# Performance work log

Hardware: AMD Instinct MI355X
Metric: run time of the kernel (lower is better)

The kernel has to match this reference:

```python
import jax, jax.numpy as jnp
import numpy as np
import math

LIMBS = [(5, 7), (7, 9), (6, 8), (8, 10), (11, 13), (13, 15), (12, 14), (14, 16), (5, 6), (11, 12), (5, 11), (6, 12), (5, 12), (6, 11)]
PARENT = jnp.array([l[0] for l in LIMBS], dtype=jnp.int32)
CHILD = jnp.array([l[1] for l in LIMBS], dtype=jnp.int32)
EXPECTED_2D_LEN = 0.15

B = 65536
D_MODEL = 64
HID = 128


def _ln(x, g, b, eps=1e-5):
    m = jnp.mean(x, axis=-1, keepdims=True)
    v = jnp.mean(jnp.square(x - m), axis=-1, keepdims=True)
    return (x - m) * jax.lax.rsqrt(v + eps) * g + b


def _unit(x, eps=1e-6):
    # F.normalize semantics: divide by max(norm, eps)
    n = jnp.linalg.norm(x, axis=-1, keepdims=True)
    return x / jnp.maximum(n, eps)


def setup_inputs() -> dict:
    key = jax.random.key(0)
    ks = jax.random.split(key, 32)
    d = {}
    d["joint_features"] = jax.random.normal(ks[0], (B, 17, D_MODEL), jnp.float32)
    d["pose_2d"] = jax.random.normal(ks[1], (B, 17, 2), jnp.float32)
    d["pose_3d"] = jax.random.normal(ks[2], (B, 17, 3), jnp.float32)
    d["azimuth"] = jax.random.uniform(ks[3], (B,), jnp.float32) * 360.0
    d["elevation"] = jax.random.uniform(ks[4], (B,), jnp.float32) * 180.0 - 90.0
    d["projected_2d"] = jax.random.normal(ks[5], (B, 17, 2), jnp.float32)

    def lin(k, out_f, in_f, std=None):
        s = std if std is not None else 1.0 / math.sqrt(in_f)
        return jax.random.normal(k, (out_f, in_f), jnp.float32) * s

    # current_orient_encoder: Linear(3->32), LayerNorm(32), ReLU
    d["co_w"] = lin(ks[6], HID // 4, 3)
    d["co_b"] = jnp.zeros((HID // 4,), jnp.float32)
    d["co_g"] = jnp.ones((HID // 4,), jnp.float32)
    d["co_be"] = jnp.zeros((HID // 4,), jnp.float32)
    # limb_2d_encoder: Linear(4->64), LayerNorm(64), ReLU
    d["l2_w"] = lin(ks[7], HID // 2, 4)
    d["l2_b"] = jnp.zeros((HID // 2,), jnp.float32)
    d["l2_g"] = jnp.ones((HID // 2,), jnp.float32)
    d["l2_be"] = jnp.zeros((HID // 2,), jnp.float32)
    # view_encoder: Linear(7->32), ReLU
    d["v_w"] = lin(ks[8], HID // 4, 7)
    d["v_b"] = jnp.zeros((HID // 4,), jnp.float32)
    # limb_head: Linear(256->128), LN(128), LeakyReLU, Linear(128->128), LeakyReLU, Linear(128->3)
    in_dim = HID // 2 + HID // 4 + D_MODEL * 2 + HID // 4  # 256
    d["h1_w"] = lin(ks[9], HID, in_dim)
    d["h1_b"] = jnp.zeros((HID,), jnp.float32)
    d["h_g"] = jnp.ones((HID,), jnp.float32)
    d["h_be"] = jnp.zeros((HID,), jnp.float32)
    d["h2_w"] = lin(ks[10], HID, HID)
    d["h2_b"] = jnp.zeros((HID,), jnp.float32)
    d["h3_w"] = lin(ks[11], 3, HID, std=0.01)
    d["h3_b"] = jnp.zeros((3,), jnp.float32)
    return d


def reference(joint_features, pose_2d, pose_3d, azimuth, elevation, projected_2d,
              co_w, co_b, co_g, co_be, l2_w, l2_b, l2_g, l2_be, v_w, v_b,
              h1_w, h1_b, h_g, h_be, h2_w, h2_b, h3_w, h3_b):
    nl = PARENT.shape[0]  # 14
    # gather parent/child joint features: (B, 14, d_model)
    pf = joint_features[:, PARENT, :]
    cf = joint_features[:, CHILD, :]
    # current 3D orientations from input pose
    cur = _unit(pose_3d[:, CHILD, :] - pose_3d[:, PARENT, :])  # (B,14,3)
    co = jax.nn.relu(_ln(jnp.einsum('blk,ok->blo', cur, co_w) + co_b, co_g, co_be))
    # view encoder from azimuth/elevation
    az = azimuth * (math.pi / 180.0)
    el = elevation * (math.pi / 180.0)
    sa, ca, se, ce = jnp.sin(az), jnp.cos(az), jnp.sin(el), jnp.cos(el)
    view_in = jnp.stack([sa * ce, se, ca * ce, sa, ca, se, ce], axis=-1)  # (B,7)
    vf = jax.nn.relu(view_in @ v_w.T + v_b)  # (B,32)
    vf = jnp.broadcast_to(vf[:, None, :], (vf.shape[0], nl, vf.shape[-1]))
    # 2D foreshortening features from projected_2d
    v2 = projected_2d[:, CHILD, :] - projected_2d[:, PARENT, :]  # (B,14,2)
    L = jnp.linalg.norm(v2, axis=-1, keepdims=True)
    d2 = v2 / (L + 1e-6)
    ratio = L / (EXPECTED_2D_LEN + 1e-6)
    feat2d = jnp.concatenate([d2, L, ratio], axis=-1)  # (B,14,4)
    l2 = jax.nn.relu(_ln(jnp.einsum('blk,ok->blo', feat2d, l2_w) + l2_b, l2_g, l2_be))
    # concat all branches: (B,14,256)
    lf = jnp.concatenate([l2, co, pf, cf, vf], axis=-1)
    # 3-layer MLP head
    h = jax.nn.leaky_relu(_ln(jnp.einsum('blk,ok->blo', lf, h1_w) + h1_b, h_g, h_be), 0.2)
    h = jax.nn.leaky_relu(jnp.einsum('blk,ok->blo', h, h2_w) + h2_b, 0.2)
    delta = jnp.einsum('blk,ok->blo', h, h3_w) + h3_b  # (B,14,3)
    return _unit(cur + delta)
```

## Files before the change

kernel.cpp:

```cpp
#include <hip/hip_runtime.h>


#define NTHR   1024
#define NBLK   256
#define NTILES 14336
#define C2D    6.66662222251852f
#define RAD    0.017453292519943295f

typedef __bf16 bf16x8 __attribute__((ext_vector_type(8)));
typedef __bf16 bf16x4 __attribute__((ext_vector_type(4)));
typedef float  f32x4  __attribute__((ext_vector_type(4)));

#define PARENT_PK 0x10106097863120ull
#define CHILD_PK  0x677671b9a85342ull

__global__ __launch_bounds__(256) void prep_kernel(
    const float* __restrict__ w1, const float* __restrict__ w2,
    __bf16* __restrict__ wsb)
{
  const int u = blockIdx.x * 256 + threadIdx.x;
  if (u < 4096) {
    const int lane = u & 63, t = u >> 6;
    const int f = t & 1, kk = (t >> 1) & 7, wn = t >> 4;
    const int col = wn * 32 + f * 16 + (lane & 15);
    const int kb  = kk * 32 + (lane >> 4) * 8;
    __bf16* dst = wsb + (size_t)u * 8;
    #pragma unroll
    for (int j = 0; j < 8; ++j) dst[j] = (__bf16)w1[col * 256 + kb + j];
  } else if (u < 6144) {
    const int v = u - 4096;
    const int lane = v & 63, t = v >> 6;
    const int f = t & 1, kk = (t >> 1) & 3, wn = t >> 3;
    const int col = wn * 32 + f * 16 + (lane & 15);
    const int kb  = kk * 32 + (lane >> 4) * 8;
    __bf16* dst = wsb + 32768 + (size_t)v * 8;
    #pragma unroll
    for (int j = 0; j < 8; ++j) dst[j] = (__bf16)w2[col * 128 + kb + j];
  }
}

struct Smem {
  __bf16 w1f[32768];
  __bf16 w2f[16384];
  __bf16 lf[64][264];
  __bf16 h [64][132];
  f32x4  scal4[256];
  float  w3c[384];
  float  h1b[128], hg[128], hbe[128], h2b[128];
  float  partG1[512];
  float  partG2[768];
};

__device__ __forceinline__ float RFL(float x) {
  return __uint_as_float((unsigned)__builtin_amdgcn_readfirstlane((int)__float_as_uint(x)));
}

__global__ __launch_bounds__(NTHR, 4) void limb_kernel(
    const float* __restrict__ jf,  const float* __restrict__ p3g,
    const float* __restrict__ az,  const float* __restrict__ el,
    const float* __restrict__ p2d,
    const float* __restrict__ cow, const float* __restrict__ cob,
    const float* __restrict__ cog, const float* __restrict__ cobe,
    const float* __restrict__ l2w, const float* __restrict__ l2b,
    const float* __restrict__ l2g, const float* __restrict__ l2be,
    const float* __restrict__ vw,  const float* __restrict__ vb,
    const float* __restrict__ h1bg, const float* __restrict__ hgg,
    const float* __restrict__ hbeg, const float* __restrict__ h2bg,
    const float* __restrict__ w3,  const float* __restrict__ h3bg,
    const __bf16* __restrict__ wsb,
    float* __restrict__ out)
{
  __shared__ Smem sm;
  const int tid  = threadIdx.x;
  const int wave = tid >> 6;
  const int lane = tid & 63;
  const int lrow = lane & 15, lk8 = lane >> 4;
  const int mp = wave >> 2, nt = wave & 3;
  const int nrow = nt * 16 + lrow;
  const int cb0 = mp * 32 + lk8 * 4;
  const int cb1 = cb0 + 16;
  const int myrow0 = wave * 4;

  {
    const uint4* s1 = (const uint4*)wsb;
    uint4* d1 = (uint4*)sm.w1f;
    for (int i = tid; i < 4096; i += NTHR) d1[i] = s1[i];
    const uint4* s2 = (const uint4*)(wsb + 32768);
    uint4* d2 = (uint4*)sm.w2f;
    for (int i = tid; i < 2048; i += NTHR) d2[i] = s2[i];
  }
  if (tid < 384) sm.w3c[tid] = w3[tid];
  if (tid < 128) {
    sm.h1b[tid] = h1bg[tid]; sm.hg[tid] = hgg[tid];
    sm.hbe[tid] = hbeg[tid]; sm.h2b[tid] = h2bg[tid];
  }
  const float h3b0 = h3bg[0], h3b1 = h3bg[1], h3b2 = h3bg[2];

  float lQxx, lQxy2, lQxz2, lQyy, lQyz2, lQzz, lrx2, lry2, lrz2, ls0;
  float lmx, lmy, lmz, lmb;
  {
    float s1x = 0, s1y = 0, s1z = 0, sb = 0;
    float sxx = 0, sxy = 0, sxz = 0, syy = 0, syz = 0, szz = 0;
    float sbx = 0, sby = 0, sbz = 0, sbb = 0;
    for (int o = 0; o < 64; ++o) {
      const float w0 = l2w[o * 4 + 0], w1v = l2w[o * 4 + 1];
      const float w2v = l2w[o * 4 + 2] + C2D * l2w[o * 4 + 3];
      const float bo = l2b[o];
      s1x += w0; s1y += w1v; s1z += w2v; sb += bo;
      sxx += w0 * w0; sxy += w0 * w1v; sxz += w0 * w2v;
      syy += w1v * w1v; syz += w1v * w2v; szz += w2v * w2v;
      sbx += w0 * bo; sby += w1v * bo; sbz += w2v * bo; sbb += bo * bo;
    }
    const float i = 1.f / 64.f;
    lmx = RFL(s1x * i); lmy = RFL(s1y * i); lmz = RFL(s1z * i); lmb = RFL(sb * i);
    lQxx = RFL(sxx * i - lmx * lmx); lQxy2 = RFL(2.f * (sxy * i - lmx * lmy));
    lQxz2 = RFL(2.f * (sxz * i - lmx * lmz)); lQyy = RFL(syy * i - lmy * lmy);
    lQyz2 = RFL(2.f * (syz * i - lmy * lmz)); lQzz = RFL(szz * i - lmz * lmz);
    lrx2 = RFL(2.f * (sbx * i - lmx * lmb)); lry2 = RFL(2.f * (sby * i - lmy * lmb));
    lrz2 = RFL(2.f * (sbz * i - lmz * lmb)); ls0 = RFL(sbb * i - lmb * lmb);
  }
  float cQxx, cQxy2, cQxz2, cQyy, cQyz2, cQzz, crx2, cry2, crz2, cs0;
  float cmx, cmy, cmz, cmb;
  {
    float s1x = 0, s1y = 0, s1z = 0, sb = 0;
    float sxx = 0, sxy = 0, sxz = 0, syy = 0, syz = 0, szz = 0;
    float sbx = 0, sby = 0, sbz = 0, sbb = 0;
    for (int o = 0; o < 32; ++o) {
      const float w0 = cow[o * 3 + 0], w1v = cow[o * 3 + 1], w2v = cow[o * 3 + 2];
      const float bo = cob[o];
      s1x += w0; s1y += w1v; s1z += w2v; sb += bo;
      sxx += w0 * w0; sxy += w0 * w1v; sxz += w0 * w2v;
      syy += w1v * w1v; syz += w1v * w2v; szz += w2v * w2v;
      sbx += w0 * bo; sby += w1v * bo; sbz += w2v * bo; sbb += bo * bo;
    }
    const float i = 1.f / 32.f;
    cmx = RFL(s1x * i); cmy = RFL(s1y * i); cmz = RFL(s1z * i); cmb = RFL(sb * i);
    cQxx = RFL(sxx * i - cmx * cmx); cQxy2 = RFL(2.f * (sxy * i - cmx * cmy));
    cQxz2 = RFL(2.f * (sxz * i - cmx * cmz)); cQyy = RFL(syy * i - cmy * cmy);
    cQyz2 = RFL(2.f * (syz * i - cmy * cmz)); cQzz = RFL(szz * i - cmz * cmz);
    crx2 = RFL(2.f * (sbx * i - cmx * cmb)); cry2 = RFL(2.f * (sby * i - cmy * cmb));
    crz2 = RFL(2.f * (sbz * i - cmz * cmb)); cs0 = RFL(sbb * i - cmb * cmb);
  }

  const float lwc0 = l2w[lane * 4 + 0] - lmx;
  const float lwc1 = l2w[lane * 4 + 1] - lmy;
  const float lwc2 = (l2w[lane * 4 + 2] + C2D * l2w[lane * 4 + 3]) - lmz;
  const float lbc  = l2b[lane] - lmb;
  const float lgv  = l2g[lane], lbev = l2be[lane];
  float u0, u1, u2, u3, u4, u5, u6;
  if (lane < 32) {
    u0 = cow[lane * 3 + 0] - cmx; u1 = cow[lane * 3 + 1] - cmy;
    u2 = cow[lane * 3 + 2] - cmz; u3 = cob[lane] - cmb;
    u4 = cog[lane]; u5 = cobe[lane]; u6 = 0.f;
  } else {
    const int o = lane - 32;
    u0 = vw[o * 7 + 0]; u1 = vw[o * 7 + 1] + vw[o * 7 + 5];
    u2 = vw[o * 7 + 2]; u3 = vw[o * 7 + 3];
    u4 = vw[o * 7 + 4]; u5 = vw[o * 7 + 6]; u6 = vb[o];
  }

  auto jf_src = [&](int rg0x, int round) -> const float* {
    const int task = wave * 8 + round * 4 + lk8;
    const int row = task >> 1, half = task & 1;
    const unsigned rg = (unsigned)(rg0x + row);
    const unsigned b = rg / 14u;
    const int l = (int)(rg - b * 14u);
    const int j = half ? 5 + (int)((CHILD_PK >> (4 * l)) & 15ull)
                       : 5 + (int)((PARENT_PK >> (4 * l)) & 15ull);
    return jf + ((size_t)b * 17 + (size_t)j) * 64 + lrow * 4;
  };
  auto jf_store = [&](int round, float4 v) {
    const int task = wave * 8 + round * 4 + lk8;
    const int row = task >> 1, half = task & 1;
    bf16x4 o; o[0] = (__bf16)v.x; o[1] = (__bf16)v.y; o[2] = (__bf16)v.z; o[3] = (__bf16)v.w;
    *(bf16x4*)&sm.lf[row][(half ? 160 : 96) + lrow * 4] = o;
  };
  struct G12 { float p3p0, p3p1, p3p2, p3c0, p3c1, p3c2, q2p0, q2p1, q2c0, q2c1, sazv, selv; };
  auto gather12_row = [&](int rgl) -> G12 {
    G12 g;
    const unsigned rg = (unsigned)rgl;
    const unsigned b = rg / 14u;
    const int l = (int)(rg - b * 14u);
    const int p = 5 + (int)((PARENT_PK >> (4 * l)) & 15ull);
    const int c = 5 + (int)((CHILD_PK  >> (4 * l)) & 15ull);
    const float* p3 = p3g + (size_t)b * 51;
    g.p3p0 = p3[p * 3 + 0]; g.p3p1 = p3[p * 3 + 1]; g.p3p2 = p3[p * 3 + 2];
    g.p3c0 = p3[c * 3 + 0]; g.p3c1 = p3[c * 3 + 1]; g.p3c2 = p3[c * 3 + 2];
    const float* q2 = p2d + (size_t)b * 34;
    g.q2p0 = q2[p * 2 + 0]; g.q2p1 = q2[p * 2 + 1];
    g.q2c0 = q2[c * 2 + 0]; g.q2c1 = q2[c * 2 + 1];
    g.sazv = az[b]; g.selv = el[b];
    return g;
  };
  auto scal_write = [&](int row, const G12& g) {
    const float dx = g.p3c0 - g.p3p0, dy = g.p3c1 - g.p3p1, dz = g.p3c2 - g.p3p2;
    const float ci = 1.f / fmaxf(sqrtf(dx * dx + dy * dy + dz * dz), 1e-6f);
    const float cx = dx * ci, cy = dy * ci, cz = dz * ci;
    const float vx = g.q2c0 - g.q2p0, vy = g.q2c1 - g.q2p1;
    const float L  = sqrtf(vx * vx + vy * vy);
    const float il = 1.f / (L + 1e-6f);
    const float f0 = vx * il, f1 = vy * il;
    const float azr = g.sazv * RAD, elr = g.selv * RAD;
    const float sa = __sinf(azr), ca = __cosf(azr);
    const float se = __sinf(elr), ce = __cosf(elr);
    const float vl = lQxx * f0 * f0 + lQyy * f1 * f1 + lQzz * L * L +
                     lQxy2 * f0 * f1 + lQxz2 * f0 * L + lQyz2 * f1 * L +
                     lrx2 * f0 + lry2 * f1 + lrz2 * L + ls0;
    const float vc = cQxx * cx * cx + cQyy * cy * cy + cQzz * cz * cz +
                     cQxy2 * cx * cy + cQxz2 * cx * cz + cQyz2 * cy * cz +
                     crx2 * cx + cry2 * cy + crz2 * cz + cs0;
    f32x4 s0; s0[0] = cx; s0[1] = cy; s0[2] = cz; s0[3] = f0;
    f32x4 s1; s1[0] = f1; s1[1] = L; s1[2] = rsqrtf(vl + 1e-5f); s1[3] = rsqrtf(vc + 1e-5f);
    f32x4 s2; s2[0] = sa * ce; s2[1] = se; s2[2] = ca * ce; s2[3] = sa;
    f32x4 s3; s3[0] = ca; s3[1] = ce; s3[2] = 0.f; s3[3] = 0.f;
    sm.scal4[row * 4 + 0] = s0; sm.scal4[row * 4 + 1] = s1;
    sm.scal4[row * 4 + 2] = s2; sm.scal4[row * 4 + 3] = s3;
  };
  auto expandB = [&]() {
    #pragma unroll
    for (int rr = 0; rr < 4; ++rr) {
      const int row = myrow0 + rr;
      const f32x4 s0 = sm.scal4[row * 4 + 0];
      const f32x4 s1 = sm.scal4[row * 4 + 1];
      const f32x4 s2 = sm.scal4[row * 4 + 2];
      const f32x4 s3 = sm.scal4[row * 4 + 3];
      {
        const float a = lwc0 * s0[3] + lwc1 * s1[0] + lwc2 * s1[1] + lbc;
        sm.lf[row][lane] = (__bf16)fmaxf(a * s1[2] * lgv + lbev, 0.f);
      }
      if (lane < 32) {
        const float a = u0 * s0[0] + u1 * s0[1] + u2 * s0[2] + u3;
        sm.lf[row][64 + lane] = (__bf16)fmaxf(a * s1[3] * u4 + u5, 0.f);
      } else {
        const float a = u0 * s2[0] + u1 * s2[1] + u2 * s2[2] + u3 * s2[3] +
                        u4 * s3[0] + u5 * s3[1] + u6;
        sm.lf[row][224 + (lane - 32)] = (__bf16)fmaxf(a, 0.f);
      }
    }
  };

  {
    const int rg0 = blockIdx.x * 64;
    jf_store(0, *(const float4*)jf_src(rg0, 0));
    jf_store(1, *(const float4*)jf_src(rg0, 1));
    if (lane < 4) scal_write(myrow0 + lane, gather12_row(rg0 + myrow0 + lane));
    expandB();
  }
  __syncthreads();

  float curx = 0.f, cury = 0.f, curz = 0.f;
  int prevT = -1;

  for (int tile = blockIdx.x; tile < NTILES; tile += NBLK) {
    const int ntile = tile + NBLK;
    const bool pv = ntile < NTILES;

    float4 jva = {0.f, 0.f, 0.f, 0.f}, jvb = jva;
    G12 g = {};
    if (pv) {
      jva = *(const float4*)jf_src(ntile * 64, 0);
      jvb = *(const float4*)jf_src(ntile * 64, 1);
      if (lane < 4) g = gather12_row(ntile * 64 + myrow0 + lane);
    }
    if (prevT >= 0 && lane < 4) {
      const int r = myrow0 + lane;
      const f32x4 q0 = *(const f32x4*)&sm.partG2[r * 12];
      const f32x4 q1 = *(const f32x4*)&sm.partG2[r * 12 + 4];
      const f32x4 q2 = *(const f32x4*)&sm.partG2[r * 12 + 8];
      const float ox = curx + q0[0] + q0[1] + q0[2] + q0[3] + h3b0;
      const float oy = cury + q1[0] + q1[1] + q1[2] + q1[3] + h3b1;
      const float oz = curz + q2[0] + q2[1] + q2[2] + q2[3] + h3b2;
      const float nn = sqrtf(ox * ox + oy * oy + oz * oz);
      const float iv = 1.f / fmaxf(nn, 1e-6f);
      const size_t o0 = (size_t)(prevT * 64 + r) * 3;
      out[o0 + 0] = ox * iv; out[o0 + 1] = oy * iv; out[o0 + 2] = oz * iv;
    }
    f32x4 a0 = {0.f, 0.f, 0.f, 0.f}, a1 = a0;
    #pragma unroll
    for (int kk = 0; kk < 8; ++kk) {
      const bf16x8 fb  = *(const bf16x8*)&sm.lf[nrow][kk * 32 + lk8 * 8];
      const bf16x8 fa0 = *(const bf16x8*)&sm.w1f[(((mp * 8 + kk) * 2 + 0) * 64 + lane) * 8];
      const bf16x8 fa1 = *(const bf16x8*)&sm.w1f[(((mp * 8 + kk) * 2 + 1) * 64 + lane) * 8];
      a0 = __builtin_amdgcn_mfma_f32_16x16x32_bf16(fa0, fb, a0, 0, 0, 0);
      a1 = __builtin_amdgcn_mfma_f32_16x16x32_bf16(fa1, fb, a1, 0, 0, 0);
    }
    const f32x4 hb0 = *(const f32x4*)&sm.h1b[cb0];
    const f32x4 hb1 = *(const f32x4*)&sm.h1b[cb1];
    float v0[4], v1[4], ss = 0.f, qq = 0.f;
    #pragma unroll
    for (int j = 0; j < 4; ++j) {
      v0[j] = a0[j] + hb0[j]; v1[j] = a1[j] + hb1[j];
      ss += v0[j] + v1[j];
      qq = fmaf(v0[j], v0[j], qq); qq = fmaf(v1[j], v1[j], qq);
    }
    ss += __shfl_xor(ss, 16, 64); ss += __shfl_xor(ss, 32, 64);
    qq += __shfl_xor(qq, 16, 64); qq += __shfl_xor(qq, 32, 64);
    if (lk8 == 0) *(float2*)&sm.partG1[nrow * 8 + mp * 2] = make_float2(ss, qq);
    __syncthreads();

    {
      const f32x4 pa = *(const f32x4*)&sm.partG1[nrow * 8];
      const f32x4 pb = *(const f32x4*)&sm.partG1[nrow * 8 + 4];
      const float mean = (pa[0] + pa[2] + pb[0] + pb[2]) * (1.f / 128.f);
      const float var  = (pa[1] + pa[3] + pb[1] + pb[3]) * (1.f / 128.f) - mean * mean;
      const float rs = rsqrtf(var + 1e-5f);
      const f32x4 g0 = *(const f32x4*)&sm.hg[cb0],  g1 = *(const f32x4*)&sm.hg[cb1];
      const f32x4 e0 = *(const f32x4*)&sm.hbe[cb0], e1 = *(const f32x4*)&sm.hbe[cb1];
      bf16x4 y0, y1;
      #pragma unroll
      for (int j = 0; j < 4; ++j) {
        float t0 = (v0[j] - mean) * rs * g0[j] + e0[j]; t0 = (t0 > 0.f) ? t0 : 0.2f * t0;
        float t1 = (v1[j] - mean) * rs * g1[j] + e1[j]; t1 = (t1 > 0.f) ? t1 : 0.2f * t1;
        y0[j] = (__bf16)t0; y1[j] = (__bf16)t1;
      }
      *(bf16x4*)&sm.h[nrow][cb0] = y0;
      *(bf16x4*)&sm.h[nrow][cb1] = y1;
    }
    __syncthreads();

    f32x4 d0 = {0.f, 0.f, 0.f, 0.f}, d1 = d0;
    #pragma unroll
    for (int kk = 0; kk < 4; ++kk) {
      const bf16x8 fbh = *(const bf16x8*)&sm.h[nrow][kk * 32 + lk8 * 8];
      const bf16x8 fa0 = *(const bf16x8*)&sm.w2f[(((mp * 4 + kk) * 2 + 0) * 64 + lane) * 8];
      const bf16x8 fa1 = *(const bf16x8*)&sm.w2f[(((mp * 4 + kk) * 2 + 1) * 64 + lane) * 8];
      d0 = __builtin_amdgcn_mfma_f32_16x16x32_bf16(fa0, fbh, d0, 0, 0, 0);
      d1 = __builtin_amdgcn_mfma_f32_16x16x32_bf16(fa1, fbh, d1, 0, 0, 0);
    }
    if (pv) { jf_store(0, jva); jf_store(1, jvb); }
    if (lane < 4) {
      const f32x4 cu = sm.scal4[(myrow0 + lane) * 4];
      curx = cu[0]; cury = cu[1]; curz = cu[2];
      if (pv) scal_write(myrow0 + lane, g);
    }
    {
      const f32x4 b20 = *(const f32x4*)&sm.h2b[cb0], b21 = *(const f32x4*)&sm.h2b[cb1];
      const f32x4 wx0 = *(const f32x4*)&sm.w3c[cb0],        wx1 = *(const f32x4*)&sm.w3c[cb1];
      const f32x4 wy0 = *(const f32x4*)&sm.w3c[128 + cb0],  wy1 = *(const f32x4*)&sm.w3c[128 + cb1];
      const f32x4 wz0 = *(const f32x4*)&sm.w3c[256 + cb0],  wz1 = *(const f32x4*)&sm.w3c[256 + cb1];
      float p0 = 0.f, p1 = 0.f, p2 = 0.f;
      #pragma unroll
      for (int j = 0; j < 4; ++j) {
        float x0 = d0[j] + b20[j]; x0 = (x0 > 0.f) ? x0 : 0.2f * x0;
        float x1 = d1[j] + b21[j]; x1 = (x1 > 0.f) ? x1 : 0.2f * x1;
        p0 = fmaf(x0, wx0[j], fmaf(x1, wx1[j], p0));
        p1 = fmaf(x0, wy0[j], fmaf(x1, wy1[j], p1));
        p2 = fmaf(x0, wz0[j], fmaf(x1, wz1[j], p2));
      }
      p0 += __shfl_xor(p0, 16, 64); p0 += __shfl_xor(p0, 32, 64);
      p1 += __shfl_xor(p1, 16, 64); p1 += __shfl_xor(p1, 32, 64);
      p2 += __shfl_xor(p2, 16, 64); p2 += __shfl_xor(p2, 32, 64);
      if (lk8 == 0) {
        sm.partG2[nrow * 12 + 0 + mp] = p0;
        sm.partG2[nrow * 12 + 4 + mp] = p1;
        sm.partG2[nrow * 12 + 8 + mp] = p2;
      }
    }
    if (pv) expandB();
    __syncthreads();
    prevT = tile;
  }

  if (lane < 4) {
    const int r = myrow0 + lane;
    const f32x4 q0 = *(const f32x4*)&sm.partG2[r * 12];
    const f32x4 q1 = *(const f32x4*)&sm.partG2[r * 12 + 4];
    const f32x4 q2 = *(const f32x4*)&sm.partG2[r * 12 + 8];
    const float ox = curx + q0[0] + q0[1] + q0[2] + q0[3] + h3b0;
    const float oy = cury + q1[0] + q1[1] + q1[2] + q1[3] + h3b1;
    const float oz = curz + q2[0] + q2[1] + q2[2] + q2[3] + h3b2;
    const float nn = sqrtf(ox * ox + oy * oy + oz * oz);
    const float iv = 1.f / fmaxf(nn, 1e-6f);
    const size_t o0 = (size_t)(prevT * 64 + r) * 3;
    out[o0 + 0] = ox * iv; out[o0 + 1] = oy * iv; out[o0 + 2] = oz * iv;
  }
}

extern "C" void kernel_launch(void* const* d_in, const int* in_sizes, int n_in,
                              void* d_out, int out_size, void* d_ws, size_t ws_size,
                              hipStream_t stream) {
  (void)in_sizes; (void)n_in; (void)out_size; (void)ws_size;
  const float* jf   = (const float*)d_in[0];
  const float* p3   = (const float*)d_in[2];
  const float* az   = (const float*)d_in[3];
  const float* el   = (const float*)d_in[4];
  const float* p2d  = (const float*)d_in[5];
  const float* cow  = (const float*)d_in[6];
  const float* cob  = (const float*)d_in[7];
  const float* cog  = (const float*)d_in[8];
  const float* cobe = (const float*)d_in[9];
  const float* l2w  = (const float*)d_in[10];
  const float* l2b  = (const float*)d_in[11];
  const float* l2g  = (const float*)d_in[12];
  const float* l2be = (const float*)d_in[13];
  const float* vw   = (const float*)d_in[14];
  const float* vb   = (const float*)d_in[15];
  const float* w1   = (const float*)d_in[16];
  const float* h1b  = (const float*)d_in[17];
  const float* hg   = (const float*)d_in[18];
  const float* hbe  = (const float*)d_in[19];
  const float* w2   = (const float*)d_in[20];
  const float* h2b  = (const float*)d_in[21];
  const float* w3   = (const float*)d_in[22];
  const float* h3b  = (const float*)d_in[23];

  __bf16* wsb = (__bf16*)d_ws;

  prep_kernel<<<dim3(24), dim3(256), 0, stream>>>(w1, w2, wsb);
  limb_kernel<<<dim3(NBLK), dim3(NTHR), 0, stream>>>(
      jf, p3, az, el, p2d, cow, cob, cog, cobe,
      l2w, l2b, l2g, l2be, vw, vb,
      h1b, hg, hbe, h2b, w3, h3b, wsb, (float*)d_out);
}
```

Measured before the change: 343.2 us.

## Precompute per-row scalar features in a separate kernel and stream them in

Adds two pre-kernels. One reduces the LayerNorm weight statistics into closed-form quadratic coefficients. The other computes, for every (batch, limb) row, the normalized 3D direction, 2D foreshortening features, LayerNorm inverse std and view trig terms, and writes them to workspace. The main kernel then loads these 64-byte records in place of gathering pose data and doing trig inside its prefetch path. This shortens the serialized scalar work in the big kernel, at the cost of an extra full pass writing and reading about 58 MB through global memory, and it falls back to the old path when the workspace is too small.

Measured after the change: 316.5 us. 7.8% less time.

```diff
diff --git a/kernel.cpp b/kernel.cpp
--- a/kernel.cpp
+++ b/kernel.cpp
@@ -4,8 +4,11 @@
 #define NTHR   1024
 #define NBLK   256
 #define NTILES 14336
+#define NROWS  917504
 #define C2D    6.66662222251852f
 #define RAD    0.017453292519943295f
+#define WS_STAT_OFF 98304
+#define WS_SCAL_OFF 131072
 
 typedef __bf16 bf16x8 __attribute__((ext_vector_type(8)));
 typedef __bf16 bf16x4 __attribute__((ext_vector_type(4)));
@@ -39,6 +42,87 @@
   }
 }
 
+__global__ __launch_bounds__(64) void prep0_kernel(
+    const float* __restrict__ cow, const float* __restrict__ cob,
+    const float* __restrict__ l2w, const float* __restrict__ l2b,
+    float* __restrict__ statg)
+{
+  const int o = threadIdx.x;
+  const float w0 = l2w[o * 4 + 0], w1v = l2w[o * 4 + 1];
+  const float w2v = l2w[o * 4 + 2] + C2D * l2w[o * 4 + 3];
+  const float bo = l2b[o];
+  float v[14] = { w0, w1v, w2v, bo, w0 * w0, w0 * w1v, w0 * w2v,
+                  w1v * w1v, w1v * w2v, w2v * w2v, w0 * bo, w1v * bo, w2v * bo, bo * bo };
+  float c0 = 0.f, c1 = 0.f, c2 = 0.f, cb = 0.f;
+  if (o < 32) { c0 = cow[o * 3 + 0]; c1 = cow[o * 3 + 1]; c2 = cow[o * 3 + 2]; cb = cob[o]; }
+  float u[14] = { c0, c1, c2, cb, c0 * c0, c0 * c1, c0 * c2,
+                  c1 * c1, c1 * c2, c2 * c2, c0 * cb, c1 * cb, c2 * cb, cb * cb };
+  #pragma unroll
+  for (int k = 0; k < 14; ++k) {
+    #pragma unroll
+    for (int m = 1; m < 64; m <<= 1) { v[k] += __shfl_xor(v[k], m, 64); u[k] += __shfl_xor(u[k], m, 64); }
+  }
+  if (o == 0) {
+    const float i64 = 1.f / 64.f, i32 = 1.f / 32.f;
+    const float lmx = v[0] * i64, lmy = v[1] * i64, lmz = v[2] * i64, lmb = v[3] * i64;
+    statg[0] = lmx; statg[1] = lmy; statg[2] = lmz; statg[3] = lmb;
+    statg[4] = v[4] * i64 - lmx * lmx;        statg[5] = 2.f * (v[5] * i64 - lmx * lmy);
+    statg[6] = 2.f * (v[6] * i64 - lmx * lmz); statg[7] = v[7] * i64 - lmy * lmy;
+    statg[8] = 2.f * (v[8] * i64 - lmy * lmz); statg[9] = v[9] * i64 - lmz * lmz;
+    statg[10] = 2.f * (v[10] * i64 - lmx * lmb); statg[11] = 2.f * (v[11] * i64 - lmy * lmb);
+    statg[12] = 2.f * (v[12] * i64 - lmz * lmb); statg[13] = v[13] * i64 - lmb * lmb;
+    const float cmx = u[0] * i32, cmy = u[1] * i32, cmz = u[2] * i32, cmb = u[3] * i32;
+    statg[14] = cmx; statg[15] = cmy; statg[16] = cmz; statg[17] = cmb;
+    statg[18] = u[4] * i32 - cmx * cmx;        statg[19] = 2.f * (u[5] * i32 - cmx * cmy);
+    statg[20] = 2.f * (u[6] * i32 - cmx * cmz); statg[21] = u[7] * i32 - cmy * cmy;
+    statg[22] = 2.f * (u[8] * i32 - cmy * cmz); statg[23] = u[9] * i32 - cmz * cmz;
+    statg[24] = 2.f * (u[10] * i32 - cmx * cmb); statg[25] = 2.f * (u[11] * i32 - cmy * cmb);
+    statg[26] = 2.f * (u[12] * i32 - cmz * cmb); statg[27] = u[13] * i32 - cmb * cmb;
+  }
+}
+
+__global__ __launch_bounds__(256) void prep2_kernel(
+    const float* __restrict__ p3g, const float* __restrict__ az,
+    const float* __restrict__ el,  const float* __restrict__ p2d,
+    const float* __restrict__ statg, f32x4* __restrict__ scalg)
+{
+  const int r = blockIdx.x * 256 + threadIdx.x;
+  const unsigned rg = (unsigned)r;
+  const unsigned b = rg / 14u;
+  const int l = (int)(rg - b * 14u);
+  const int p = 5 + (int)((PARENT_PK >> (4 * l)) & 15ull);
+  const int c = 5 + (int)((CHILD_PK  >> (4 * l)) & 15ull);
+  const float* p3 = p3g + (size_t)b * 51;
+  const float dx = p3[c * 3 + 0] - p3[p * 3 + 0];
+  const float dy = p3[c * 3 + 1] - p3[p * 3 + 1];
+  const float dz = p3[c * 3 + 2] - p3[p * 3 + 2];
+  const float* q2 = p2d + (size_t)b * 34;
+  const float vx = q2[c * 2 + 0] - q2[p * 2 + 0];
+  const float vy = q2[c * 2 + 1] - q2[p * 2 + 1];
+  const float sazv = az[b], selv = el[b];
+
+  const float ci = 1.f / fmaxf(sqrtf(dx * dx + dy * dy + dz * dz), 1e-6f);
+  const float cx = dx * ci, cy = dy * ci, cz = dz * ci;
+  const float L  = sqrtf(vx * vx + vy * vy);
+  const float il = 1.f / (L + 1e-6f);
+  const float f0 = vx * il, f1 = vy * il;
+  const float azr = sazv * RAD, elr = selv * RAD;
+  const float sa = __sinf(azr), ca = __cosf(azr);
+  const float se = __sinf(elr), ce = __cosf(elr);
+  const float vl = statg[4] * f0 * f0 + statg[7] * f1 * f1 + statg[9] * L * L +
+                   statg[5] * f0 * f1 + statg[6] * f0 * L + statg[8] * f1 * L +
+                   statg[10] * f0 + statg[11] * f1 + statg[12] * L + statg[13];
+  const float vc = statg[18] * cx * cx + statg[21] * cy * cy + statg[23] * cz * cz +
+                   statg[19] * cx * cy + statg[20] * cx * cz + statg[22] * cy * cz +
+                   statg[24] * cx + statg[25] * cy + statg[26] * cz + statg[27];
+  f32x4 s0; s0[0] = cx; s0[1] = cy; s0[2] = cz; s0[3] = f0;
+  f32x4 s1; s1[0] = f1; s1[1] = L; s1[2] = rsqrtf(vl + 1e-5f); s1[3] = rsqrtf(vc + 1e-5f);
+  f32x4 s2; s2[0] = sa * ce; s2[1] = se; s2[2] = ca * ce; s2[3] = sa;
+  f32x4 s3; s3[0] = ca; s3[1] = ce; s3[2] = 0.f; s3[3] = 0.f;
+  scalg[(size_t)r * 4 + 0] = s0; scalg[(size_t)r * 4 + 1] = s1;
+  scalg[(size_t)r * 4 + 2] = s2; scalg[(size_t)r * 4 + 3] = s3;
+}
+
 struct Smem {
   __bf16 w1f[32768];
   __bf16 w2f[16384];
@@ -55,6 +139,7 @@
   return __uint_as_float((unsigned)__builtin_amdgcn_readfirstlane((int)__float_as_uint(x)));
 }
 
+template<bool PRECOMP>
 __global__ __launch_bounds__(NTHR, 4) void limb_kernel(
     const float* __restrict__ jf,  const float* __restrict__ p3g,
     const float* __restrict__ az,  const float* __restrict__ el,
@@ -67,7 +152,7 @@
     const float* __restrict__ h1bg, const float* __restrict__ hgg,
     const float* __restrict__ hbeg, const float* __restrict__ h2bg,
     const float* __restrict__ w3,  const float* __restrict__ h3bg,
-    const __bf16* __restrict__ wsb,
+    const __bf16* __restrict__ wsb, const f32x4* __restrict__ scalg,
     float* __restrict__ out)
 {
   __shared__ Smem sm;
@@ -243,7 +328,17 @@
     const int rg0 = blockIdx.x * 64;
     jf_store(0, *(const float4*)jf_src(rg0, 0));
     jf_store(1, *(const float4*)jf_src(rg0, 1));
-    if (lane < 4) scal_write(myrow0 + lane, gather12_row(rg0 + myrow0 + lane));
+    if (lane < 4) {
+      if (PRECOMP) {
+        const f32x4* sp = scalg + (size_t)(rg0 + myrow0 + lane) * 4;
+        sm.scal4[(myrow0 + lane) * 4 + 0] = sp[0];
+        sm.scal4[(myrow0 + lane) * 4 + 1] = sp[1];
+        sm.scal4[(myrow0 + lane) * 4 + 2] = sp[2];
+        sm.scal4[(myrow0 + lane) * 4 + 3] = sp[3];
+      } else {
+        scal_write(myrow0 + lane, gather12_row(rg0 + myrow0 + lane));
+      }
+    }
     expandB();
   }
   __syncthreads();
@@ -256,11 +351,19 @@
     const bool pv = ntile < NTILES;
 
     float4 jva = {0.f, 0.f, 0.f, 0.f}, jvb = jva;
+    f32x4 s0n = {0.f, 0.f, 0.f, 0.f}, s1n = s0n, s2n = s0n, s3n = s0n;
     G12 g = {};
     if (pv) {
       jva = *(const float4*)jf_src(ntile * 64, 0);
       jvb = *(const float4*)jf_src(ntile * 64, 1);
-      if (lane < 4) g = gather12_row(ntile * 64 + myrow0 + lane);
+      if (lane < 4) {
+        if (PRECOMP) {
+          const f32x4* sp = scalg + (size_t)(ntile * 64 + myrow0 + lane) * 4;
+          s0n = sp[0]; s1n = sp[1]; s2n = sp[2]; s3n = sp[3];
+        } else {
+          g = gather12_row(ntile * 64 + myrow0 + lane);
+        }
+      }
     }
     if (prevT >= 0 && lane < 4) {
       const int r = myrow0 + lane;
@@ -331,7 +434,16 @@
     if (lane < 4) {
       const f32x4 cu = sm.scal4[(myrow0 + lane) * 4];
       curx = cu[0]; cury = cu[1]; curz = cu[2];
-      if (pv) scal_write(myrow0 + lane, g);
+      if (pv) {
+        if (PRECOMP) {
+          sm.scal4[(myrow0 + lane) * 4 + 0] = s0n;
+          sm.scal4[(myrow0 + lane) * 4 + 1] = s1n;
+          sm.scal4[(myrow0 + lane) * 4 + 2] = s2n;
+          sm.scal4[(myrow0 + lane) * 4 + 3] = s3n;
+        } else {
+          scal_write(myrow0 + lane, g);
+        }
+      }
     }
     {
       const f32x4 b20 = *(const f32x4*)&sm.h2b[cb0], b21 = *(const f32x4*)&sm.h2b[cb1];
@@ -379,7 +491,7 @@
 extern "C" void kernel_launch(void* const* d_in, const int* in_sizes, int n_in,
                               void* d_out, int out_size, void* d_ws, size_t ws_size,
                               hipStream_t stream) {
-  (void)in_sizes; (void)n_in; (void)out_size; (void)ws_size;
+  (void)in_sizes; (void)n_in; (void)out_size;
   const float* jf   = (const float*)d_in[0];
   const float* p3   = (const float*)d_in[2];
   const float* az   = (const float*)d_in[3];
@@ -404,11 +516,25 @@
   const float* w3   = (const float*)d_in[22];
   const float* h3b  = (const float*)d_in[23];
 
-  __bf16* wsb = (__bf16*)d_ws;
+  __bf16* wsb   = (__bf16*)d_ws;
+  float*  statg = (float*)((char*)d_ws + WS_STAT_OFF);
+  f32x4*  scalg = (f32x4*)((char*)d_ws + WS_SCAL_OFF);
+
+  const size_t ws_need = (size_t)WS_SCAL_OFF + (size_t)NROWS * 64;
+  const bool pre = ws_size >= ws_need;
 
   prep_kernel<<<dim3(24), dim3(256), 0, stream>>>(w1, w2, wsb);
-  limb_kernel<<<dim3(NBLK), dim3(NTHR), 0, stream>>>(
-      jf, p3, az, el, p2d, cow, cob, cog, cobe,
-      l2w, l2b, l2g, l2be, vw, vb,
-      h1b, hg, hbe, h2b, w3, h3b, wsb, (float*)d_out);
+  if (pre) {
+    prep0_kernel<<<dim3(1), dim3(64), 0, stream>>>(cow, cob, l2w, l2b, statg);
+    prep2_kernel<<<dim3(NROWS / 256), dim3(256), 0, stream>>>(p3, az, el, p2d, statg, scalg);
+    limb_kernel<true><<<dim3(NBLK), dim3(NTHR), 0, stream>>>(
+        jf, p3, az, el, p2d, cow, cob, cog, cobe,
+        l2w, l2b, l2g, l2be, vw, vb,
+        h1b, hg, hbe, h2b, w3, h3b, wsb, scalg, (float*)d_out);
+  } else {
+    limb_kernel<false><<<dim3(NBLK), dim3(NTHR), 0, stream>>>(
+        jf, p3, az, el, p2d, cow, cob, cog, cobe,
+        l2w, l2b, l2g, l2be, vw, vb,
+        h1b, hg, hbe, h2b, w3, h3b, wsb, scalg, (float*)d_out);
+  }
 }
```
